# Performance work log

Measured on AMD Instinct MI355X. Metric: run time of the kernel, lower is better.

The kernel has to match this reference:

```python
import jax, jax.numpy as jnp
import numpy as np

NUM_HEADS = 8
NUM_POINTS = 4


def setup_inputs() -> dict:
    key = jax.random.key(0)
    ks = jax.random.split(key, 10)
    B, H, W, D = 8, 64, 64, 256
    N = H * W
    nh, P = NUM_HEADS, NUM_POINTS

    def xavier(k, shape):
        fan_in, fan_out = shape[0], shape[1]
        lim = float(np.sqrt(6.0 / (fan_in + fan_out)))
        return jax.random.uniform(k, shape, jnp.float32, -lim, lim)

    x = jax.random.normal(ks[0], (B, N, D), jnp.float32)
    qkv_w = xavier(ks[1], (D, 3 * D))
    qkv_b = jnp.zeros((3 * D,), jnp.float32)
    # offset network is zero-init in the module; use small random weights so the
    # deformable sampling is actually exercised (offsets nonzero).
    off_w = jax.random.normal(ks[2], (D, nh * P * 2), jnp.float32) * 0.01
    off_b = jnp.zeros((nh * P * 2,), jnp.float32)
    attw_w = xavier(ks[3], (D, nh * P))
    attw_b = jnp.zeros((nh * P,), jnp.float32)
    proj_w = xavier(ks[4], (D, D))
    proj_b = jnp.zeros((D,), jnp.float32)
    return {
        "x": x, "qkv_w": qkv_w, "qkv_b": qkv_b,
        "off_w": off_w, "off_b": off_b,
        "attw_w": attw_w, "attw_b": attw_b,
        "proj_w": proj_w, "proj_b": proj_b,
        "H": 64, "W": 64,
    }


def _deformable_forward(x, qkv_w, qkv_b, off_w, off_b, attw_w, attw_b, proj_w, proj_b, H, W):
    B, N, D = x.shape
    nh, P = NUM_HEADS, NUM_POINTS
    hd = D // nh

    qkv = x @ qkv_w + qkv_b                      # [B,N,3D] (q,k computed but unused, as in the original)
    v = qkv[..., 2 * D:].reshape(B, N, nh, hd)   # [B,N,nh,hd]

    offsets = jnp.tanh((x @ off_w + off_b).reshape(B, N, nh, P, 2)) * 2.0

    ys, xs = jnp.meshgrid(jnp.arange(H, dtype=x.dtype), jnp.arange(W, dtype=x.dtype), indexing="ij")
    ref = jnp.stack([xs, ys], axis=-1).reshape(N, 2)          # [N,2] (x,y) pixel coords
    loc = ref[None, :, None, None, :] + offsets               # [B,N,nh,P,2] pixel coords
    # (module normalizes to [-1,1] then grid_sample align_corners=True un-normalizes
    #  back to exactly these pixel coordinates, so we sample at `loc` directly)

    # value as flat spatial map per head: [B,nh,hd,N], n = y*W + x
    vf = v.transpose(0, 2, 3, 1).reshape(B, nh, hd, N)

    gx, gy = loc[..., 0], loc[..., 1]
    x0 = jnp.floor(gx); y0 = jnp.floor(gy)
    x1 = x0 + 1.0;      y1 = y0 + 1.0
    wx1 = gx - x0; wx0 = 1.0 - wx1
    wy1 = gy - y0; wy0 = 1.0 - wy1

    def corner(xi, yi, w):
        # bilinear corner with zeros padding: zero weight if corner out of bounds
        valid = (xi >= 0) & (xi < W) & (yi >= 0) & (yi < H)
        idx = (jnp.clip(yi, 0, H - 1) * W + jnp.clip(xi, 0, W - 1)).astype(jnp.int32)
        idx2 = idx.transpose(0, 2, 1, 3).reshape(B, nh, N * P)          # [B,nh,N*P]
        g = jnp.take_along_axis(vf, idx2[:, :, None, :], axis=3)        # [B,nh,hd,N*P]
        w2 = (w * valid.astype(x.dtype)).transpose(0, 2, 1, 3).reshape(B, nh, 1, N * P)
        return g * w2

    sampled = (corner(x0, y0, wx0 * wy0) + corner(x1, y0, wx1 * wy0)
               + corner(x0, y1, wx0 * wy1) + corner(x1, y1, wx1 * wy1))
    sampled = sampled.reshape(B, nh, hd, N, P)

    attn = jax.nn.softmax((x @ attw_w + attw_b).reshape(B, N, nh, P), axis=-1)
    out = jnp.einsum("bhcnp,bnhp->bnhc", sampled, attn).reshape(B, N, D)
    return out @ proj_w + proj_b


def reference(x, qkv_w, qkv_b, off_w, off_b, attw_w, attw_b, proj_w, proj_b, H, W):
    return _deformable_forward(x, qkv_w, qkv_b, off_w, off_b, attw_w, attw_b, proj_w, proj_b, H, W)
```

## Files before the change

### kernel.cpp

```cpp
#include <hip/hip_runtime.h>
#include <hip/hip_bf16.h>
#include <cmath>

#define NN 4096
typedef __attribute__((ext_vector_type(8))) short short8;
typedef __attribute__((ext_vector_type(4))) float f32x4;

__device__ __forceinline__ float bf2f(unsigned short u) {
  union { unsigned int i; float f; } c; c.i = ((unsigned int)u) << 16; return c.f;
}

__global__ __launch_bounds__(256) void cvt_w(
    const float* __restrict__ qkv_w, const float* __restrict__ off_w,
    const float* __restrict__ attw_w, const float* __restrict__ proj_w,
    __hip_bfloat16* __restrict__ wcatT, __hip_bfloat16* __restrict__ pjT)
{
  const int t = threadIdx.x;
  if (blockIdx.x < 256) {
    int k = blockIdx.x;
    wcatT[t * 256 + k] = __float2bfloat16(qkv_w[k * 768 + 512 + t]);
    if (t < 128) {
      int c2 = 256 + t;
      float v = 0.f;
      if (c2 < 320)      v = off_w[k * 64 + (c2 - 256)];
      else if (c2 < 352) v = attw_w[k * 32 + (c2 - 320)];
      wcatT[c2 * 256 + k] = __float2bfloat16(v);
    }
  } else {
    int k = blockIdx.x - 256;
    pjT[t * 256 + k] = __float2bfloat16(proj_w[k * 256 + t]);
  }
}

__global__ __launch_bounds__(512) void gemm_voff(
    const float* __restrict__ x,
    const __hip_bfloat16* __restrict__ wcatT,
    const float* __restrict__ vbias,
    const float* __restrict__ off_b, const float* __restrict__ attw_b,
    __hip_bfloat16* __restrict__ vb,
    unsigned int* __restrict__ table)
{
  __shared__ float smemf[12800];
  short* As = (short*)smemf;
  short* Bs = As + 128 * 40;
  float (*L)[100] = (float(*)[100])smemf;

  const int t = threadIdx.x;
  const int bid = blockIdx.x;
  const int m0 = (((bid & 7) << 5) | (bid >> 3)) * 128;
  const int wave = t >> 6, lane = t & 63, q = lane >> 4, ln = lane & 15;
  const int wm = (wave & 1) * 64, wn = (wave >> 1) * 96;

  f32x4 acc[4][6] = {};

  const int arow = t >> 2, aseg = t & 3;
  const float* apg = x + (size_t)(m0 + arow) * 256 + aseg * 8;

  for (int k0 = 0; k0 < 256; k0 += 32) {
    float4 f0 = *(const float4*)(apg + k0);
    float4 f1 = *(const float4*)(apg + k0 + 4);
    alignas(16) __hip_bfloat16 cv[8] = {
      __float2bfloat16(f0.x), __float2bfloat16(f0.y), __float2bfloat16(f0.z), __float2bfloat16(f0.w),
      __float2bfloat16(f1.x), __float2bfloat16(f1.y), __float2bfloat16(f1.z), __float2bfloat16(f1.w)};
    *(int4*)&As[arow * 40 + aseg * 8] = *(int4*)cv;
#pragma unroll
    for (int i = 0; i < 3; ++i) {
      int u = t + i * 512;
      int brow = u >> 2, bseg = u & 3;
      *(int4*)&Bs[brow * 40 + bseg * 8] =
          *(const int4*)&wcatT[(size_t)brow * 256 + k0 + bseg * 8];
    }
    __syncthreads();
    short8 a[4], b[6];
#pragma unroll
    for (int i = 0; i < 4; ++i) a[i] = *(const short8*)&As[(wm + i * 16 + ln) * 40 + q * 8];
#pragma unroll
    for (int j = 0; j < 6; ++j) b[j] = *(const short8*)&Bs[(wn + j * 16 + ln) * 40 + q * 8];
#pragma unroll
    for (int i = 0; i < 4; ++i)
#pragma unroll
      for (int j = 0; j < 6; ++j)
        acc[i][j] = __builtin_amdgcn_mfma_f32_16x16x32_bf16(a[i], b[j], acc[i][j], 0, 0, 0);
    __syncthreads();
  }

#pragma unroll
  for (int j = 0; j < 6; ++j) {
    int col = wn + j * 16 + ln;
    if (col < 256) {
      float bv = vbias[col];
#pragma unroll
      for (int i = 0; i < 4; ++i) {
        int rowb = m0 + wm + i * 16 + q * 4;
#pragma unroll
        for (int r = 0; r < 4; ++r)
          vb[(size_t)(rowb + r) * 256 + col] = __float2bfloat16(acc[i][j][r] + bv);
      }
    } else if (col < 352) {
      int lc = col - 256;
      float bv = (lc < 64) ? off_b[lc] : attw_b[lc - 64];
#pragma unroll
      for (int i = 0; i < 4; ++i)
#pragma unroll
        for (int r = 0; r < 4; ++r)
          L[wm + i * 16 + q * 4 + r][lc] = acc[i][j][r] + bv;
    }
  }
  __syncthreads();

#pragma unroll
  for (int it = 0; it < 2; ++it) {
    int pl = t + it * 512;
    int rr = pl >> 3, h = pl & 7;
    int row = m0 + rr;
    int nl = row & (NN - 1);
    float refx = (float)(nl & 63);
    float refy = (float)(nl >> 6);

    float a0 = L[rr][64 + h * 4 + 0], a1 = L[rr][64 + h * 4 + 1];
    float a2 = L[rr][64 + h * 4 + 2], a3 = L[rr][64 + h * 4 + 3];
    float mx = fmaxf(fmaxf(a0, a1), fmaxf(a2, a3));
    float e0 = expf(a0 - mx), e1 = expf(a1 - mx), e2 = expf(a2 - mx), e3 = expf(a3 - mx);
    float inv = 1.f / (e0 + e1 + e2 + e3);
    float at[4] = {e0 * inv, e1 * inv, e2 * inv, e3 * inv};

    alignas(16) unsigned short idxs[16];
    alignas(16) _Float16 wsv[16];
#pragma unroll
    for (int p = 0; p < 4; ++p) {
      float gx = refx + 2.f * tanhf(L[rr][h * 8 + p * 2 + 0]);
      float gy = refy + 2.f * tanhf(L[rr][h * 8 + p * 2 + 1]);
      float x0f = floorf(gx), y0f = floorf(gy);
      int x0 = (int)x0f, y0 = (int)y0f;
      int x1 = x0 + 1,   y1 = y0 + 1;
      float wx1 = gx - x0f, wx0 = 1.f - wx1;
      float wy1 = gy - y0f, wy0 = 1.f - wy1;
      int cx0 = min(max(x0, 0), 63), cx1 = min(max(x1, 0), 63);
      int cy0 = min(max(y0, 0), 63), cy1 = min(max(y1, 0), 63);
      float vx0 = (x0 >= 0 && x0 <= 63) ? 1.f : 0.f;
      float vx1 = (x1 >= 0 && x1 <= 63) ? 1.f : 0.f;
      float vy0 = (y0 >= 0 && y0 <= 63) ? 1.f : 0.f;
      float vy1 = (y1 >= 0 && y1 <= 63) ? 1.f : 0.f;
      float ap = at[p];
      idxs[p * 4 + 0] = (unsigned short)(cy0 * 64 + cx0);
      idxs[p * 4 + 1] = (unsigned short)(cy0 * 64 + cx1);
      idxs[p * 4 + 2] = (unsigned short)(cy1 * 64 + cx0);
      idxs[p * 4 + 3] = (unsigned short)(cy1 * 64 + cx1);
      wsv[p * 4 + 0] = (_Float16)(ap * wx0 * wy0 * vx0 * vy0);
      wsv[p * 4 + 1] = (_Float16)(ap * wx1 * wy0 * vx1 * vy0);
      wsv[p * 4 + 2] = (_Float16)(ap * wx0 * wy1 * vx0 * vy1);
      wsv[p * 4 + 3] = (_Float16)(ap * wx1 * wy1 * vx1 * vy1);
    }
    uint4* dst = (uint4*)(table + ((size_t)row * 8 + h) * 16);
    dst[0] = *(uint4*)&idxs[0];
    dst[1] = *(uint4*)&idxs[8];
    dst[2] = *(uint4*)&wsv[0];
    dst[3] = *(uint4*)&wsv[8];
  }
}

__global__ __launch_bounds__(256) void sample_kernel(
    const __hip_bfloat16* __restrict__ v,
    const unsigned int* __restrict__ table,
    __hip_bfloat16* __restrict__ y)
{
  __shared__ uint4 Tab[256];
  const int t = threadIdx.x;
  const int bid = blockIdx.x;
  const int p0 = (((bid & 7) << 9) | (bid >> 3)) * 64;
  Tab[t] = *(const uint4*)(table + (size_t)p0 * 16 + t * 4);
  __syncthreads();

  const int g = t & 3, p = t >> 2;
  const int pg = p0 + p;
  const int h = pg & 7;
  const int row = pg >> 3;
  const int b = row >> 12;
  const unsigned short* ip = (const unsigned short*)&Tab[p * 4];
  const _Float16* wp = (const _Float16*)((const char*)&Tab[p * 4] + 32);
  const char* vbase = (const char*)(v + (size_t)b * NN * 256 + h * 32 + g * 8);

  float acc[8] = {};
#pragma unroll
  for (int j = 0; j < 16; ++j) {
    float w = (float)wp[j];
    int idx = ip[j];
    int4 pk = *(const int4*)(vbase + (size_t)idx * 512);
    const unsigned short* u = (const unsigned short*)&pk;
#pragma unroll
    for (int c = 0; c < 8; ++c) acc[c] += w * bf2f(u[c]);
  }
  alignas(16) __hip_bfloat16 o[8];
#pragma unroll
  for (int c = 0; c < 8; ++c) o[c] = __float2bfloat16(acc[c]);
  *(int4*)((char*)y + ((size_t)row * 256 + h * 32 + g * 8) * 2) = *(int4*)o;
}

__global__ __launch_bounds__(256) void gemm_proj(
    const short* __restrict__ A, const short* __restrict__ BT,
    const float* __restrict__ bias, float* __restrict__ out)
{
  __shared__ short As[128 * 40];
  __shared__ short Bs[128 * 40];
  const int t = threadIdx.x;
  const int bid = blockIdx.x;
  const int local = bid >> 3;
  const int n0 = (local & 1) * 128;
  const int m0 = (((bid & 7) << 5) | (local >> 1)) * 128;
  const int wave = t >> 6, lane = t & 63, q = lane >> 4, ln = lane & 15;
  const int wm = (wave & 1) * 64, wn = (wave >> 1) * 64;

  f32x4 acc[4][4] = {};

  for (int k0 = 0; k0 < 256; k0 += 32) {
#pragma unroll
    for (int u = 0; u < 2; ++u) {
      int c = t + u * 256;
      int row = c >> 2, kq = c & 3;
      *(int4*)&As[row * 40 + kq * 8] =
          *(const int4*)&A[(size_t)(m0 + row) * 256 + k0 + kq * 8];
      *(int4*)&Bs[row * 40 + kq * 8] =
          *(const int4*)&BT[(size_t)(n0 + row) * 256 + k0 + kq * 8];
    }
    __syncthreads();
    short8 a[4], b[4];
#pragma unroll
    for (int i = 0; i < 4; ++i) a[i] = *(const short8*)&As[(wm + i * 16 + ln) * 40 + q * 8];
#pragma unroll
    for (int j = 0; j < 4; ++j) b[j] = *(const short8*)&Bs[(wn + j * 16 + ln) * 40 + q * 8];
#pragma unroll
    for (int i = 0; i < 4; ++i)
#pragma unroll
      for (int j = 0; j < 4; ++j)
        acc[i][j] = __builtin_amdgcn_mfma_f32_16x16x32_bf16(a[i], b[j], acc[i][j], 0, 0, 0);
    __syncthreads();
  }

#pragma unroll
  for (int j = 0; j < 4; ++j) {
    int col = n0 + wn + j * 16 + ln;
    float bv = bias[col];
#pragma unroll
    for (int i = 0; i < 4; ++i) {
      int rowb = m0 + wm + i * 16 + q * 4;
#pragma unroll
      for (int r = 0; r < 4; ++r)
        out[(size_t)(rowb + r) * 256 + col] = acc[i][j][r] + bv;
    }
  }
}

extern "C" void kernel_launch(void* const* d_in, const int* in_sizes, int n_in,
                              void* d_out, int out_size, void* d_ws, size_t ws_size,
                              hipStream_t stream) {
  const float* x      = (const float*)d_in[0];
  const float* qkv_w  = (const float*)d_in[1];
  const float* qkv_b  = (const float*)d_in[2];
  const float* off_w  = (const float*)d_in[3];
  const float* off_b  = (const float*)d_in[4];
  const float* attw_w = (const float*)d_in[5];
  const float* attw_b = (const float*)d_in[6];
  const float* proj_w = (const float*)d_in[7];
  const float* proj_b = (const float*)d_in[8];
  float* out = (float*)d_out;

  char* ws = (char*)d_ws;
  __hip_bfloat16* vb    = (__hip_bfloat16*)(ws);
  __hip_bfloat16* yb    = (__hip_bfloat16*)(ws + 16777216);
  unsigned int*   table = (unsigned int*)  (ws + 33554432);
  __hip_bfloat16* wcatT = (__hip_bfloat16*)(ws + 50331648);
  __hip_bfloat16* pjT   = (__hip_bfloat16*)(ws + 50528256);

  cvt_w<<<512, 256, 0, stream>>>(qkv_w, off_w, attw_w, proj_w, wcatT, pjT);
  gemm_voff<<<256, 512, 0, stream>>>(x, wcatT, qkv_b + 512, off_b, attw_b, vb, table);
  sample_kernel<<<4096, 256, 0, stream>>>(vb, table, yb);
  gemm_proj<<<512, 256, 0, stream>>>((const short*)yb, (const short*)pjT, proj_b, out);
}
```

Measured before the change: 148.1 us.

## Store compact fp16 offsets/attention in table, compute bilinear taps in sampler; retile proj GEMM

The offset/attention table no longer holds precomputed corner indices and weights (64 bytes per point-head). It now stores only fp16 tanh offsets and softmax weights (24 bytes, padded to 32). The sample kernel recomputes the bilinear corner indices and weights itself, which cuts table write and read traffic but duplicates that arithmetic across the 4 threads sharing a point-head. Offsets stored in fp16 lose some precision near large reference coordinates. Separately, the projection GEMM switches to 64x256 tiles so each block covers the full N dimension, which changes B-tile reuse and the grid shape.

Result: faster. 142.5 us (-3.8%).

```diff
diff --git a/kernel.cpp b/kernel.cpp
--- a/kernel.cpp
+++ b/kernel.cpp
@@ -113,49 +113,27 @@
     int pl = t + it * 512;
     int rr = pl >> 3, h = pl & 7;
     int row = m0 + rr;
-    int nl = row & (NN - 1);
-    float refx = (float)(nl & 63);
-    float refy = (float)(nl >> 6);
 
     float a0 = L[rr][64 + h * 4 + 0], a1 = L[rr][64 + h * 4 + 1];
     float a2 = L[rr][64 + h * 4 + 2], a3 = L[rr][64 + h * 4 + 3];
     float mx = fmaxf(fmaxf(a0, a1), fmaxf(a2, a3));
     float e0 = expf(a0 - mx), e1 = expf(a1 - mx), e2 = expf(a2 - mx), e3 = expf(a3 - mx);
     float inv = 1.f / (e0 + e1 + e2 + e3);
-    float at[4] = {e0 * inv, e1 * inv, e2 * inv, e3 * inv};
-
-    alignas(16) unsigned short idxs[16];
-    alignas(16) _Float16 wsv[16];
+
+    alignas(16) _Float16 pk[12];
 #pragma unroll
     for (int p = 0; p < 4; ++p) {
-      float gx = refx + 2.f * tanhf(L[rr][h * 8 + p * 2 + 0]);
-      float gy = refy + 2.f * tanhf(L[rr][h * 8 + p * 2 + 1]);
-      float x0f = floorf(gx), y0f = floorf(gy);
-      int x0 = (int)x0f, y0 = (int)y0f;
-      int x1 = x0 + 1,   y1 = y0 + 1;
-      float wx1 = gx - x0f, wx0 = 1.f - wx1;
-      float wy1 = gy - y0f, wy0 = 1.f - wy1;
-      int cx0 = min(max(x0, 0), 63), cx1 = min(max(x1, 0), 63);
-      int cy0 = min(max(y0, 0), 63), cy1 = min(max(y1, 0), 63);
-      float vx0 = (x0 >= 0 && x0 <= 63) ? 1.f : 0.f;
-      float vx1 = (x1 >= 0 && x1 <= 63) ? 1.f : 0.f;
-      float vy0 = (y0 >= 0 && y0 <= 63) ? 1.f : 0.f;
-      float vy1 = (y1 >= 0 && y1 <= 63) ? 1.f : 0.f;
-      float ap = at[p];
-      idxs[p * 4 + 0] = (unsigned short)(cy0 * 64 + cx0);
-      idxs[p * 4 + 1] = (unsigned short)(cy0 * 64 + cx1);
-      idxs[p * 4 + 2] = (unsigned short)(cy1 * 64 + cx0);
-      idxs[p * 4 + 3] = (unsigned short)(cy1 * 64 + cx1);
-      wsv[p * 4 + 0] = (_Float16)(ap * wx0 * wy0 * vx0 * vy0);
-      wsv[p * 4 + 1] = (_Float16)(ap * wx1 * wy0 * vx1 * vy0);
-      wsv[p * 4 + 2] = (_Float16)(ap * wx0 * wy1 * vx0 * vy1);
-      wsv[p * 4 + 3] = (_Float16)(ap * wx1 * wy1 * vx1 * vy1);
-    }
-    uint4* dst = (uint4*)(table + ((size_t)row * 8 + h) * 16);
-    dst[0] = *(uint4*)&idxs[0];
-    dst[1] = *(uint4*)&idxs[8];
-    dst[2] = *(uint4*)&wsv[0];
-    dst[3] = *(uint4*)&wsv[8];
+      pk[p * 2 + 0] = (_Float16)(2.f * tanhf(L[rr][h * 8 + p * 2 + 0]));
+      pk[p * 2 + 1] = (_Float16)(2.f * tanhf(L[rr][h * 8 + p * 2 + 1]));
+    }
+    pk[8]  = (_Float16)(e0 * inv);
+    pk[9]  = (_Float16)(e1 * inv);
+    pk[10] = (_Float16)(e2 * inv);
+    pk[11] = (_Float16)(e3 * inv);
+
+    size_t pg = (size_t)row * 8 + h;
+    *(uint4*)(table + pg * 8)     = *(uint4*)&pk[0];
+    *(uint2*)(table + pg * 8 + 4) = *(uint2*)&pk[8];
   }
 }
 
@@ -164,11 +142,11 @@
     const unsigned int* __restrict__ table,
     __hip_bfloat16* __restrict__ y)
 {
-  __shared__ uint4 Tab[256];
+  __shared__ uint4 Tab[128];
   const int t = threadIdx.x;
   const int bid = blockIdx.x;
   const int p0 = (((bid & 7) << 9) | (bid >> 3)) * 64;
-  Tab[t] = *(const uint4*)(table + (size_t)p0 * 16 + t * 4);
+  if (t < 128) Tab[t] = *(const uint4*)(table + (size_t)p0 * 8 + t * 4);
   __syncthreads();
 
   const int g = t & 3, p = t >> 2;
@@ -176,15 +154,48 @@
   const int h = pg & 7;
   const int row = pg >> 3;
   const int b = row >> 12;
-  const unsigned short* ip = (const unsigned short*)&Tab[p * 4];
-  const _Float16* wp = (const _Float16*)((const char*)&Tab[p * 4] + 32);
+  const int nl = row & (NN - 1);
+  const float refx = (float)(nl & 63);
+  const float refy = (float)(nl >> 6);
+
+  const _Float16* dp  = (const _Float16*)&Tab[p * 2];
+  const _Float16* ap_ = (const _Float16*)&Tab[p * 2 + 1];
+
+  alignas(16) unsigned short idxs[16];
+  float ws[16];
+#pragma unroll
+  for (int pp = 0; pp < 4; ++pp) {
+    float gx = refx + (float)dp[2 * pp + 0];
+    float gy = refy + (float)dp[2 * pp + 1];
+    float x0f = floorf(gx), y0f = floorf(gy);
+    int x0 = (int)x0f, y0 = (int)y0f;
+    int x1 = x0 + 1,   y1 = y0 + 1;
+    float wx1 = gx - x0f, wx0 = 1.f - wx1;
+    float wy1 = gy - y0f, wy0 = 1.f - wy1;
+    int cx0 = min(max(x0, 0), 63), cx1 = min(max(x1, 0), 63);
+    int cy0 = min(max(y0, 0), 63), cy1 = min(max(y1, 0), 63);
+    float vx0 = (x0 >= 0 && x0 <= 63) ? 1.f : 0.f;
+    float vx1 = (x1 >= 0 && x1 <= 63) ? 1.f : 0.f;
+    float vy0 = (y0 >= 0 && y0 <= 63) ? 1.f : 0.f;
+    float vy1 = (y1 >= 0 && y1 <= 63) ? 1.f : 0.f;
+    float apv = (float)ap_[pp];
+    idxs[pp * 4 + 0] = (unsigned short)(cy0 * 64 + cx0);
+    idxs[pp * 4 + 1] = (unsigned short)(cy0 * 64 + cx1);
+    idxs[pp * 4 + 2] = (unsigned short)(cy1 * 64 + cx0);
+    idxs[pp * 4 + 3] = (unsigned short)(cy1 * 64 + cx1);
+    ws[pp * 4 + 0] = apv * wx0 * wy0 * vx0 * vy0;
+    ws[pp * 4 + 1] = apv * wx1 * wy0 * vx1 * vy0;
+    ws[pp * 4 + 2] = apv * wx0 * wy1 * vx0 * vy1;
+    ws[pp * 4 + 3] = apv * wx1 * wy1 * vx1 * vy1;
+  }
+
   const char* vbase = (const char*)(v + (size_t)b * NN * 256 + h * 32 + g * 8);
 
   float acc[8] = {};
 #pragma unroll
   for (int j = 0; j < 16; ++j) {
-    float w = (float)wp[j];
-    int idx = ip[j];
+    float w = ws[j];
+    int idx = idxs[j];
     int4 pk = *(const int4*)(vbase + (size_t)idx * 512);
     const unsigned short* u = (const unsigned short*)&pk;
 #pragma unroll
@@ -200,32 +211,32 @@
     const short* __restrict__ A, const short* __restrict__ BT,
     const float* __restrict__ bias, float* __restrict__ out)
 {
-  __shared__ short As[128 * 40];
-  __shared__ short Bs[128 * 40];
+  __shared__ short As[64 * 40];
+  __shared__ short Bs[256 * 40];
   const int t = threadIdx.x;
   const int bid = blockIdx.x;
-  const int local = bid >> 3;
-  const int n0 = (local & 1) * 128;
-  const int m0 = (((bid & 7) << 5) | (local >> 1)) * 128;
+  const int m0 = (((bid & 7) << 6) | (bid >> 3)) * 64;
   const int wave = t >> 6, lane = t & 63, q = lane >> 4, ln = lane & 15;
-  const int wm = (wave & 1) * 64, wn = (wave >> 1) * 64;
+  const int wn = wave * 64;
 
   f32x4 acc[4][4] = {};
 
+  const int arow = t >> 2, aseg = t & 3;
+  const short* apg = A + (size_t)(m0 + arow) * 256 + aseg * 8;
+
   for (int k0 = 0; k0 < 256; k0 += 32) {
-#pragma unroll
-    for (int u = 0; u < 2; ++u) {
-      int c = t + u * 256;
-      int row = c >> 2, kq = c & 3;
-      *(int4*)&As[row * 40 + kq * 8] =
-          *(const int4*)&A[(size_t)(m0 + row) * 256 + k0 + kq * 8];
-      *(int4*)&Bs[row * 40 + kq * 8] =
-          *(const int4*)&BT[(size_t)(n0 + row) * 256 + k0 + kq * 8];
+    *(int4*)&As[arow * 40 + aseg * 8] = *(const int4*)(apg + k0);
+#pragma unroll
+    for (int u2 = 0; u2 < 4; ++u2) {
+      int c = t + u2 * 256;
+      int col = c >> 2, kq = c & 3;
+      *(int4*)&Bs[col * 40 + kq * 8] =
+          *(const int4*)&BT[(size_t)col * 256 + k0 + kq * 8];
     }
     __syncthreads();
     short8 a[4], b[4];
 #pragma unroll
-    for (int i = 0; i < 4; ++i) a[i] = *(const short8*)&As[(wm + i * 16 + ln) * 40 + q * 8];
+    for (int i = 0; i < 4; ++i) a[i] = *(const short8*)&As[(i * 16 + ln) * 40 + q * 8];
 #pragma unroll
     for (int j = 0; j < 4; ++j) b[j] = *(const short8*)&Bs[(wn + j * 16 + ln) * 40 + q * 8];
 #pragma unroll
@@ -238,11 +249,11 @@
 
 #pragma unroll
   for (int j = 0; j < 4; ++j) {
-    int col = n0 + wn + j * 16 + ln;
+    int col = wn + j * 16 + ln;
     float bv = bias[col];
 #pragma unroll
     for (int i = 0; i < 4; ++i) {
-      int rowb = m0 + wm + i * 16 + q * 4;
+      int rowb = m0 + i * 16 + q * 4;
 #pragma unroll
       for (int r = 0; r < 4; ++r)
         out[(size_t)(rowb + r) * 256 + col] = acc[i][j][r] + bv;
@@ -268,8 +279,8 @@
   __hip_bfloat16* vb    = (__hip_bfloat16*)(ws);
   __hip_bfloat16* yb    = (__hip_bfloat16*)(ws + 16777216);
   unsigned int*   table = (unsigned int*)  (ws + 33554432);
-  __hip_bfloat16* wcatT = (__hip_bfloat16*)(ws + 50331648);
-  __hip_bfloat16* pjT   = (__hip_bfloat16*)(ws + 50528256);
+  __hip_bfloat16* wcatT = (__hip_bfloat16*)(ws + 41943040);
+  __hip_bfloat16* pjT   = (__hip_bfloat16*)(ws + 42139648);
 
   cvt_w<<<512, 256, 0, stream>>>(qkv_w, off_w, attw_w, proj_w, wcatT, pjT);
   gemm_voff<<<256, 512, 0, stream>>>(x, wcatT, qkv_b + 512, off_b, attw_b, vb, table);
```
